# Optimization experiments

Hardware: AMD Instinct MI355X
Metric: run time of the kernel (lower is better)

The kernel has to match this reference:

```python
import jax, jax.numpy as jnp
import numpy as np

# lower-triangular <-> 3x3 symmetric matrix index maps (match torch_lotri2mat/mat2lotri)
LOTRI = np.array([[0, 1, 3], [1, 2, 4], [3, 4, 5]])
ROWS = np.array([0, 1, 1, 2, 2, 2])
COLS = np.array([0, 0, 1, 0, 1, 2])
NUM_NEWTON_ITERS = 6


def det3(A):
    # A: (N,3,3)
    return (A[:, 0, 0] * (A[:, 1, 1] * A[:, 2, 2] - A[:, 1, 2] * A[:, 2, 1])
            - A[:, 0, 1] * (A[:, 1, 0] * A[:, 2, 2] - A[:, 1, 2] * A[:, 2, 0])
            + A[:, 0, 2] * (A[:, 1, 0] * A[:, 2, 1] - A[:, 1, 1] * A[:, 2, 0]))


def inv3(A):
    # closed-form 3x3 inverse via adjugate; A: (N,3,3)
    c00 = A[:, 1, 1] * A[:, 2, 2] - A[:, 1, 2] * A[:, 2, 1]
    c01 = A[:, 0, 2] * A[:, 2, 1] - A[:, 0, 1] * A[:, 2, 2]
    c02 = A[:, 0, 1] * A[:, 1, 2] - A[:, 0, 2] * A[:, 1, 1]
    c10 = A[:, 1, 2] * A[:, 2, 0] - A[:, 1, 0] * A[:, 2, 2]
    c11 = A[:, 0, 0] * A[:, 2, 2] - A[:, 0, 2] * A[:, 2, 0]
    c12 = A[:, 0, 2] * A[:, 1, 0] - A[:, 0, 0] * A[:, 1, 2]
    c20 = A[:, 1, 0] * A[:, 2, 1] - A[:, 1, 1] * A[:, 2, 0]
    c21 = A[:, 0, 1] * A[:, 2, 0] - A[:, 0, 0] * A[:, 2, 1]
    c22 = A[:, 0, 0] * A[:, 1, 1] - A[:, 0, 1] * A[:, 1, 0]
    adj = jnp.stack([jnp.stack([c00, c01, c02], -1),
                     jnp.stack([c10, c11, c12], -1),
                     jnp.stack([c20, c21, c22], -1)], -2)  # (N,3,3)
    det = (A[:, 0, 0] * c00 + A[:, 0, 1] * c10 + A[:, 0, 2] * c20)
    return adj / det[:, None, None]


def trilinear_warp(img, ddf):
    # img: (B,C,H,W,D), ddf: (B,3,H,W,D) in voxel units; border padding (clamped corners)
    B, C, H, W, D = img.shape
    base = jnp.stack(jnp.meshgrid(jnp.arange(H), jnp.arange(W), jnp.arange(D),
                                  indexing='ij'), 0).astype(img.dtype)  # (3,H,W,D)
    coords = base[None] + ddf                                           # (B,3,H,W,D)
    c0 = jnp.floor(coords)
    frac = coords - c0
    c0i = c0.astype(jnp.int32)
    dims = jnp.array([H, W, D], jnp.int32).reshape(1, 3, 1, 1, 1)
    lo = jnp.clip(c0i, 0, dims - 1)
    hi = jnp.clip(c0i + 1, 0, dims - 1)
    imgf = img.reshape(B, C, H * W * D)

    def gather(xi, yi, zi):
        lin = (xi * W + yi) * D + zi                      # (B,H,W,D)
        idx = jnp.broadcast_to(lin.reshape(B, 1, -1), (B, C, H * W * D))
        return jnp.take_along_axis(imgf, idx, axis=2).reshape(B, C, H, W, D)

    fx, fy, fz = frac[:, 0, None], frac[:, 1, None], frac[:, 2, None]  # (B,1,H,W,D)
    x0, y0, z0 = lo[:, 0], lo[:, 1], lo[:, 2]
    x1, y1, z1 = hi[:, 0], hi[:, 1], hi[:, 2]
    out = jnp.zeros_like(img)
    for xi, wx in ((x0, 1.0 - fx), (x1, fx)):
        for yi, wy in ((y0, 1.0 - fy), (y1, fy)):
            for zi, wz in ((z0, 1.0 - fz), (z1, fz)):
                out = out + wx * wy * wz * gather(xi, yi, zi)
    return out


def ddf_jacobian(ddf):
    # Jacobian of the deformation phi(x)=x+ddf(x): J = I + d(ddf_i)/dx_j (central differences)
    rows = []
    for i in range(3):
        g = jnp.gradient(ddf[:, i], axis=(1, 2, 3))  # list of 3 arrays (B,H,W,D)
        rows.append(jnp.stack(g, axis=1))
    J = jnp.stack(rows, axis=1)                      # (B,3,3,H,W,D)
    eye = jnp.eye(3, dtype=ddf.dtype).reshape(1, 3, 3, 1, 1, 1)
    return J + eye


def newton_polar_det(X, n_iters):
    # Newton iteration for polar decomposition with determinant scaling
    U = X
    for _ in range(n_iters):
        zeta = jnp.abs(det3(U)) ** (-1.0 / 3.0)
        zU = zeta[:, None, None] * U
        U = 0.5 * (zU + inv3(jnp.swapaxes(zU, -1, -2)))
    return U


def setup_inputs() -> dict:
    key = jax.random.key(0)
    k1, k2 = jax.random.split(key)
    B, H, W, D = 2, 128, 128, 128
    dti = jax.random.normal(k1, (B, 6, H, W, D), dtype=jnp.float32)
    # smooth, realistic displacement field so J = I + grad(ddf) is well-conditioned
    g = jnp.stack(jnp.meshgrid(jnp.arange(H), jnp.arange(W), jnp.arange(D),
                               indexing='ij'), 0).astype(jnp.float32) / H  # (3,H,W,D)
    two_pi = 2.0 * jnp.pi
    amp = 2.0
    ddf = amp * jnp.stack([jnp.sin(two_pi * (g[0] + 0.5 * g[1])),
                           jnp.cos(two_pi * (g[1] + 0.5 * g[2])),
                           jnp.sin(two_pi * (g[2] + 0.5 * g[0]))], 0)  # (3,H,W,D)
    ddf = jnp.broadcast_to(ddf[None], (B, 3, H, W, D))
    ddf = ddf + 0.02 * jax.random.normal(k2, (B, 3, H, W, D), dtype=jnp.float32)
    return {"dti": dti, "ddf": ddf}


def reference(dti, ddf):
    B, _, H, W, D = dti.shape
    # 1) warp the lower-triangular DTI with trilinear interpolation (border padding)
    warped_lotri = trilinear_warp(dti, ddf)              # (B,6,H,W,D)
    # 2) lotri -> 3x3 symmetric matrices, absorb spatial dims
    Dmat = warped_lotri[:, LOTRI]                        # (B,3,3,H,W,D)
    Dns = Dmat.transpose(0, 3, 4, 5, 1, 2).reshape(-1, 3, 3)
    # 3) Jacobian of DDF, absorb spatial dims
    J = ddf_jacobian(ddf)                                # (B,3,3,H,W,D)
    Jns = J.transpose(0, 3, 4, 5, 1, 2).reshape(-1, 3, 3)
    # 4) rotation from polar decomposition (Newton, det scaling)
    R = newton_polar_det(Jns, NUM_NEWTON_ITERS)          # (N,3,3)
    # 5) finite-strain reorientation: R^T D R per voxel
    out_ns = jnp.einsum('nji,njk,nkl->nil', R, Dns, R)
    # 6) expand spatial dims, mat -> lotri
    out_mat = out_ns.reshape(B, H, W, D, 3, 3).transpose(0, 4, 5, 1, 2, 3)
    return out_mat[:, ROWS, COLS]                        # (B,6,H,W,D)
```

## Files before the change

### kernel.cpp

```cpp
#include <hip/hip_runtime.h>

#define NH 128
#define NW 128
#define ND 128
#define HWD (NH * NW * ND)
#define NB 2

__global__ __launch_bounds__(256) void warp_dti_kernel(
    const float* __restrict__ dti,
    const float* __restrict__ ddf,
    float* __restrict__ out)
{
    const int tid = blockIdx.x * 256 + threadIdx.x;
    const int d = tid & (ND - 1);
    const int w = (tid >> 7) & (NW - 1);
    const int h = (tid >> 14) & (NH - 1);
    const int b = tid >> 21;
    const int sp = tid & (HWD - 1);

    const float* dbase = ddf + b * 3 * HWD;

    float u[3];
#pragma unroll
    for (int c = 0; c < 3; ++c) u[c] = dbase[c * HWD + sp];

    float A[3][3];
#pragma unroll
    for (int c = 0; c < 3; ++c) {
        const float* p = dbase + c * HWD;
        float gh, gw, gd;
        if (h == 0)           gh = p[sp + NW * ND] - u[c];
        else if (h == NH - 1) gh = u[c] - p[sp - NW * ND];
        else                  gh = 0.5f * (p[sp + NW * ND] - p[sp - NW * ND]);
        if (w == 0)           gw = p[sp + ND] - u[c];
        else if (w == NW - 1) gw = u[c] - p[sp - ND];
        else                  gw = 0.5f * (p[sp + ND] - p[sp - ND]);
        if (d == 0)           gd = p[sp + 1] - u[c];
        else if (d == ND - 1) gd = u[c] - p[sp - 1];
        else                  gd = 0.5f * (p[sp + 1] - p[sp - 1]);
        A[c][0] = gh; A[c][1] = gw; A[c][2] = gd;
    }
    A[0][0] += 1.0f; A[1][1] += 1.0f; A[2][2] += 1.0f;

    float U[3][3];
#pragma unroll
    for (int i = 0; i < 3; ++i)
#pragma unroll
        for (int j = 0; j < 3; ++j) U[i][j] = A[i][j];

#pragma unroll
    for (int it = 0; it < 6; ++it) {
        float c00 = U[1][1]*U[2][2] - U[1][2]*U[2][1];
        float c01 = U[0][2]*U[2][1] - U[0][1]*U[2][2];
        float c02 = U[0][1]*U[1][2] - U[0][2]*U[1][1];
        float c10 = U[1][2]*U[2][0] - U[1][0]*U[2][2];
        float c11 = U[0][0]*U[2][2] - U[0][2]*U[2][0];
        float c12 = U[0][2]*U[1][0] - U[0][0]*U[1][2];
        float c20 = U[1][0]*U[2][1] - U[1][1]*U[2][0];
        float c21 = U[0][1]*U[2][0] - U[0][0]*U[2][1];
        float c22 = U[0][0]*U[1][1] - U[0][1]*U[1][0];
        float det = U[0][0]*c00 + U[0][1]*c10 + U[0][2]*c20;

        float l    = __log2f(fabsf(det));
        float zeta = __builtin_amdgcn_exp2f(-0.33333333333333333f * l);
        float s    = copysignf(zeta * zeta, det);
        float hz = 0.5f * zeta;
        float hs = 0.5f * s;

        float n00 = hz*U[0][0] + c00*hs;
        float n01 = hz*U[0][1] + c10*hs;
        float n02 = hz*U[0][2] + c20*hs;
        float n10 = hz*U[1][0] + c01*hs;
        float n11 = hz*U[1][1] + c11*hs;
        float n12 = hz*U[1][2] + c21*hs;
        float n20 = hz*U[2][0] + c02*hs;
        float n21 = hz*U[2][1] + c12*hs;
        float n22 = hz*U[2][2] + c22*hs;
        U[0][0]=n00; U[0][1]=n01; U[0][2]=n02;
        U[1][0]=n10; U[1][1]=n11; U[1][2]=n12;
        U[2][0]=n20; U[2][1]=n21; U[2][2]=n22;
    }

    float cx = (float)h + u[0];
    float cy = (float)w + u[1];
    float cz = (float)d + u[2];
    float flx = floorf(cx), fly = floorf(cy), flz = floorf(cz);
    float fx = cx - flx, fy = cy - fly, fz = cz - flz;
    int x0 = (int)flx, y0 = (int)fly, z0 = (int)flz;
    int xi[2], yi[2], zi[2];
    xi[0] = min(max(x0,     0), NH - 1); xi[1] = min(max(x0 + 1, 0), NH - 1);
    yi[0] = min(max(y0,     0), NW - 1); yi[1] = min(max(y0 + 1, 0), NW - 1);
    zi[0] = min(max(z0,     0), ND - 1); zi[1] = min(max(z0 + 1, 0), ND - 1);
    float wx[2] = {1.0f - fx, fx};
    float wy[2] = {1.0f - fy, fy};
    float wz[2] = {1.0f - fz, fz};

    const float* img = dti + b * 6 * HWD;
    float acc[6] = {0.f, 0.f, 0.f, 0.f, 0.f, 0.f};
#pragma unroll
    for (int i = 0; i < 2; ++i) {
#pragma unroll
        for (int j = 0; j < 2; ++j) {
            int rowoff = (xi[i] * NW + yi[j]) * ND;
            float wij = wx[i] * wy[j];
#pragma unroll
            for (int k = 0; k < 2; ++k) {
                float wgt = wij * wz[k];
                int lin = rowoff + zi[k];
#pragma unroll
                for (int ch = 0; ch < 6; ++ch)
                    acc[ch] += wgt * img[ch * HWD + lin];
            }
        }
    }

    float Dm[3][3];
    Dm[0][0] = acc[0]; Dm[0][1] = acc[1]; Dm[0][2] = acc[3];
    Dm[1][0] = acc[1]; Dm[1][1] = acc[2]; Dm[1][2] = acc[4];
    Dm[2][0] = acc[3]; Dm[2][1] = acc[4]; Dm[2][2] = acc[5];

    float M[3][3];
#pragma unroll
    for (int i = 0; i < 3; ++i)
#pragma unroll
        for (int k = 0; k < 3; ++k)
            M[i][k] = U[0][i]*Dm[0][k] + U[1][i]*Dm[1][k] + U[2][i]*Dm[2][k];

    float T00 = M[0][0]*U[0][0] + M[0][1]*U[1][0] + M[0][2]*U[2][0];
    float T10 = M[1][0]*U[0][0] + M[1][1]*U[1][0] + M[1][2]*U[2][0];
    float T11 = M[1][0]*U[0][1] + M[1][1]*U[1][1] + M[1][2]*U[2][1];
    float T20 = M[2][0]*U[0][0] + M[2][1]*U[1][0] + M[2][2]*U[2][0];
    float T21 = M[2][0]*U[0][1] + M[2][1]*U[1][1] + M[2][2]*U[2][1];
    float T22 = M[2][0]*U[0][2] + M[2][1]*U[1][2] + M[2][2]*U[2][2];

    float* obase = out + b * 6 * HWD + sp;
    obase[0]       = T00;
    obase[HWD]     = T10;
    obase[2 * HWD] = T11;
    obase[3 * HWD] = T20;
    obase[4 * HWD] = T21;
    obase[5 * HWD] = T22;
}

extern "C" void kernel_launch(void* const* d_in, const int* in_sizes, int n_in,
                              void* d_out, int out_size, void* d_ws, size_t ws_size,
                              hipStream_t stream) {
    const float* dti = (const float*)d_in[0];
    const float* ddf = (const float*)d_in[1];
    float* o = (float*)d_out;
    const int n = NB * HWD;
    warp_dti_kernel<<<n / 256, 256, 0, stream>>>(dti, ddf, o);
}
```

Baseline: 308.6 us.

## Issue all gathers before Newton iterations and use branchless stencil offsets

Moves the trilinear coordinate computation and all 48 DTI gathers ahead of the polar-decomposition Newton loop, fenced by a sched_barrier, so gather memory latency overlaps the ALU-heavy iterations. The boundary if/else chains in the Jacobian stencil become branchless clamped offsets with a scale factor, and index math is derived from block and thread ids separately. It costs many more live registers (48 gathered values plus stencil neighbours), which can lower occupancy.

```diff
diff --git a/kernel.cpp b/kernel.cpp
--- a/kernel.cpp
+++ b/kernel.cpp
@@ -4,6 +4,7 @@
 #define NW 128
 #define ND 128
 #define HWD (NH * NW * ND)
+#define NWD (NW * ND)
 #define NB 2
 
 __global__ __launch_bounds__(256) void warp_dti_kernel(
@@ -11,42 +12,81 @@
     const float* __restrict__ ddf,
     float* __restrict__ out)
 {
-    const int tid = blockIdx.x * 256 + threadIdx.x;
-    const int d = tid & (ND - 1);
-    const int w = (tid >> 7) & (NW - 1);
-    const int h = (tid >> 14) & (NH - 1);
-    const int b = tid >> 21;
-    const int sp = tid & (HWD - 1);
+    const int blk   = blockIdx.x;
+    const int b     = blk >> 13;
+    const int blkin = blk & 8191;
+    const int tid   = threadIdx.x;
+    const int sp    = (blkin << 8) | tid;
+    const int d     = tid & (ND - 1);
+    const int w     = ((blkin & 63) << 1) | (tid >> 7);
+    const int h     = blkin >> 6;
 
-    const float* dbase = ddf + b * 3 * HWD;
+    const int dbase = b * 3 * HWD;
 
-    float u[3];
-#pragma unroll
-    for (int c = 0; c < 3; ++c) u[c] = dbase[c * HWD + sp];
+    const int oh_m = (h > 0)      ? -NWD : 0;
+    const int oh_p = (h < NH - 1) ?  NWD : 0;
+    const int ow_m = (w > 0)      ? -ND  : 0;
+    const int ow_p = (w < NW - 1) ?  ND  : 0;
+    const int od_m = (d > 0)      ? -1   : 0;
+    const int od_p = (d < ND - 1) ?  1   : 0;
 
-    float A[3][3];
+    float uc[3], hm[3], hp[3], wm[3], wp[3], dm[3], dp[3];
 #pragma unroll
     for (int c = 0; c < 3; ++c) {
-        const float* p = dbase + c * HWD;
-        float gh, gw, gd;
-        if (h == 0)           gh = p[sp + NW * ND] - u[c];
-        else if (h == NH - 1) gh = u[c] - p[sp - NW * ND];
-        else                  gh = 0.5f * (p[sp + NW * ND] - p[sp - NW * ND]);
-        if (w == 0)           gw = p[sp + ND] - u[c];
-        else if (w == NW - 1) gw = u[c] - p[sp - ND];
-        else                  gw = 0.5f * (p[sp + ND] - p[sp - ND]);
-        if (d == 0)           gd = p[sp + 1] - u[c];
-        else if (d == ND - 1) gd = u[c] - p[sp - 1];
-        else                  gd = 0.5f * (p[sp + 1] - p[sp - 1]);
-        A[c][0] = gh; A[c][1] = gw; A[c][2] = gd;
+        const float* p = ddf + dbase + c * HWD;
+        uc[c] = p[sp];
     }
-    A[0][0] += 1.0f; A[1][1] += 1.0f; A[2][2] += 1.0f;
+#pragma unroll
+    for (int c = 0; c < 3; ++c) {
+        const float* p = ddf + dbase + c * HWD;
+        hm[c] = p[sp + oh_m];  hp[c] = p[sp + oh_p];
+        wm[c] = p[sp + ow_m];  wp[c] = p[sp + ow_p];
+        dm[c] = p[sp + od_m];  dp[c] = p[sp + od_p];
+    }
+
+    const float cx = (float)h + uc[0];
+    const float cy = (float)w + uc[1];
+    const float cz = (float)d + uc[2];
+    const float flx = floorf(cx), fly = floorf(cy), flz = floorf(cz);
+    const float fx = cx - flx, fy = cy - fly, fz = cz - flz;
+    const int x0 = (int)flx, y0 = (int)fly, z0 = (int)flz;
+    const int xa = min(max(x0,     0), NH - 1), xb = min(max(x0 + 1, 0), NH - 1);
+    const int ya = min(max(y0,     0), NW - 1), yb = min(max(y0 + 1, 0), NW - 1);
+    const int za = min(max(z0,     0), ND - 1), zb = min(max(z0 + 1, 0), ND - 1);
+
+    const int raa = (xa * NW + ya) * ND;
+    const int rab = (xa * NW + yb) * ND;
+    const int rba = (xb * NW + ya) * ND;
+    const int rbb = (xb * NW + yb) * ND;
+
+    int lin[8];
+    lin[0] = raa + za; lin[1] = raa + zb;
+    lin[2] = rab + za; lin[3] = rab + zb;
+    lin[4] = rba + za; lin[5] = rba + zb;
+    lin[6] = rbb + za; lin[7] = rbb + zb;
+
+    const int ibase = b * 6 * HWD;
+    float g[8][6];
+#pragma unroll
+    for (int c = 0; c < 8; ++c)
+#pragma unroll
+        for (int ch = 0; ch < 6; ++ch)
+            g[c][ch] = dti[ibase + ch * HWD + lin[c]];
+
+    __builtin_amdgcn_sched_barrier(0);
+
+    const float sh = (oh_m == 0 || oh_p == 0) ? 1.0f : 0.5f;
+    const float sw = (ow_m == 0 || ow_p == 0) ? 1.0f : 0.5f;
+    const float sd = (od_m == 0 || od_p == 0) ? 1.0f : 0.5f;
 
     float U[3][3];
 #pragma unroll
-    for (int i = 0; i < 3; ++i)
-#pragma unroll
-        for (int j = 0; j < 3; ++j) U[i][j] = A[i][j];
+    for (int c = 0; c < 3; ++c) {
+        U[c][0] = sh * (hp[c] - hm[c]);
+        U[c][1] = sw * (wp[c] - wm[c]);
+        U[c][2] = sd * (dp[c] - dm[c]);
+    }
+    U[0][0] += 1.0f; U[1][1] += 1.0f; U[2][2] += 1.0f;
 
 #pragma unroll
     for (int it = 0; it < 6; ++it) {
@@ -81,38 +121,19 @@
         U[2][0]=n20; U[2][1]=n21; U[2][2]=n22;
     }
 
-    float cx = (float)h + u[0];
-    float cy = (float)w + u[1];
-    float cz = (float)d + u[2];
-    float flx = floorf(cx), fly = floorf(cy), flz = floorf(cz);
-    float fx = cx - flx, fy = cy - fly, fz = cz - flz;
-    int x0 = (int)flx, y0 = (int)fly, z0 = (int)flz;
-    int xi[2], yi[2], zi[2];
-    xi[0] = min(max(x0,     0), NH - 1); xi[1] = min(max(x0 + 1, 0), NH - 1);
-    yi[0] = min(max(y0,     0), NW - 1); yi[1] = min(max(y0 + 1, 0), NW - 1);
-    zi[0] = min(max(z0,     0), ND - 1); zi[1] = min(max(z0 + 1, 0), ND - 1);
-    float wx[2] = {1.0f - fx, fx};
-    float wy[2] = {1.0f - fy, fy};
-    float wz[2] = {1.0f - fz, fz};
+    const float wxa = 1.0f - fx, wya = 1.0f - fy, wza = 1.0f - fz;
+    float wc[8];
+    wc[0] = (wxa * wya) * wza;  wc[1] = (wxa * wya) * fz;
+    wc[2] = (wxa * fy)  * wza;  wc[3] = (wxa * fy)  * fz;
+    wc[4] = (fx  * wya) * wza;  wc[5] = (fx  * wya) * fz;
+    wc[6] = (fx  * fy)  * wza;  wc[7] = (fx  * fy)  * fz;
 
-    const float* img = dti + b * 6 * HWD;
     float acc[6] = {0.f, 0.f, 0.f, 0.f, 0.f, 0.f};
 #pragma unroll
-    for (int i = 0; i < 2; ++i) {
+    for (int c = 0; c < 8; ++c)
 #pragma unroll
-        for (int j = 0; j < 2; ++j) {
-            int rowoff = (xi[i] * NW + yi[j]) * ND;
-            float wij = wx[i] * wy[j];
-#pragma unroll
-            for (int k = 0; k < 2; ++k) {
-                float wgt = wij * wz[k];
-                int lin = rowoff + zi[k];
-#pragma unroll
-                for (int ch = 0; ch < 6; ++ch)
-                    acc[ch] += wgt * img[ch * HWD + lin];
-            }
-        }
-    }
+        for (int ch = 0; ch < 6; ++ch)
+            acc[ch] = fmaf(wc[c], g[c][ch], acc[ch]);
 
     float Dm[3][3];
     Dm[0][0] = acc[0]; Dm[0][1] = acc[1]; Dm[0][2] = acc[3];
@@ -133,13 +154,13 @@
     float T21 = M[2][0]*U[0][1] + M[2][1]*U[1][1] + M[2][2]*U[2][1];
     float T22 = M[2][0]*U[0][2] + M[2][1]*U[1][2] + M[2][2]*U[2][2];
 
-    float* obase = out + b * 6 * HWD + sp;
-    obase[0]       = T00;
-    obase[HWD]     = T10;
-    obase[2 * HWD] = T11;
-    obase[3 * HWD] = T20;
-    obase[4 * HWD] = T21;
-    obase[5 * HWD] = T22;
+    const int obase = b * 6 * HWD;
+    out[obase + 0 * HWD + sp] = T00;
+    out[obase + 1 * HWD + sp] = T10;
+    out[obase + 2 * HWD + sp] = T11;
+    out[obase + 3 * HWD + sp] = T20;
+    out[obase + 4 * HWD + sp] = T21;
+    out[obase + 5 * HWD + sp] = T22;
 }
 
 extern "C" void kernel_launch(void* const* d_in, const int* in_sizes, int n_in,
```

Measured after the change: 299.3 us. 3.0% less time.

## Process two voxels per thread with software-pipelined inline-asm loads and paired z gathers

Applied to the files above, without the earlier changes.

Each thread now handles two voxels 64 planes apart in h. Global loads are issued through inline asm with manual vmcnt waits and sched barriers, so the gather for one voxel and the stencil loads for the other overlap with the Newton polar iterations. The trilinear z-pair is fetched as a single dwordx2 load, with edge-aware weights that reproduce clamping. Boundary gradients use offset and scale selection instead of branches. In exchange, register pressure rises, and the hand-set waitcnt counts are fragile if the compiler reorders or adds memory operations.

```diff
diff --git a/kernel.cpp b/kernel.cpp
--- a/kernel.cpp
+++ b/kernel.cpp
@@ -4,50 +4,17 @@
 #define NW 128
 #define ND 128
 #define HWD (NH * NW * ND)
+#define NWD (NW * ND)
 #define NB 2
 
-__global__ __launch_bounds__(256) void warp_dti_kernel(
-    const float* __restrict__ dti,
-    const float* __restrict__ ddf,
-    float* __restrict__ out)
-{
-    const int tid = blockIdx.x * 256 + threadIdx.x;
-    const int d = tid & (ND - 1);
-    const int w = (tid >> 7) & (NW - 1);
-    const int h = (tid >> 14) & (NH - 1);
-    const int b = tid >> 21;
-    const int sp = tid & (HWD - 1);
-
-    const float* dbase = ddf + b * 3 * HWD;
-
-    float u[3];
-#pragma unroll
-    for (int c = 0; c < 3; ++c) u[c] = dbase[c * HWD + sp];
-
-    float A[3][3];
-#pragma unroll
-    for (int c = 0; c < 3; ++c) {
-        const float* p = dbase + c * HWD;
-        float gh, gw, gd;
-        if (h == 0)           gh = p[sp + NW * ND] - u[c];
-        else if (h == NH - 1) gh = u[c] - p[sp - NW * ND];
-        else                  gh = 0.5f * (p[sp + NW * ND] - p[sp - NW * ND]);
-        if (w == 0)           gw = p[sp + ND] - u[c];
-        else if (w == NW - 1) gw = u[c] - p[sp - ND];
-        else                  gw = 0.5f * (p[sp + ND] - p[sp - ND]);
-        if (d == 0)           gd = p[sp + 1] - u[c];
-        else if (d == ND - 1) gd = u[c] - p[sp - 1];
-        else                  gd = 0.5f * (p[sp + 1] - p[sp - 1]);
-        A[c][0] = gh; A[c][1] = gw; A[c][2] = gd;
-    }
-    A[0][0] += 1.0f; A[1][1] += 1.0f; A[2][2] += 1.0f;
-
-    float U[3][3];
-#pragma unroll
-    for (int i = 0; i < 3; ++i)
-#pragma unroll
-        for (int j = 0; j < 3; ++j) U[i][j] = A[i][j];
-
+typedef float f32x2 __attribute__((ext_vector_type(2)));
+
+#define SB() __builtin_amdgcn_sched_barrier(0)
+#define LD1(dst, voff, base) asm volatile("global_load_dword %0, %1, %2" : "=v"(dst) : "v"(voff), "s"(base))
+#define LD2(dst, voff, base) asm volatile("global_load_dwordx2 %0, %1, %2" : "=v"(dst) : "v"(voff), "s"(base))
+#define TOUCH(x) asm volatile("" : "+v"(x))
+
+__device__ __forceinline__ void newton6(float U[3][3]) {
 #pragma unroll
     for (int it = 0; it < 6; ++it) {
         float c00 = U[1][1]*U[2][2] - U[1][2]*U[2][1];
@@ -80,66 +47,215 @@
         U[1][0]=n10; U[1][1]=n11; U[1][2]=n12;
         U[2][0]=n20; U[2][1]=n21; U[2][2]=n22;
     }
-
-    float cx = (float)h + u[0];
-    float cy = (float)w + u[1];
-    float cz = (float)d + u[2];
+}
+
+__device__ __forceinline__ void corner_setup(float cx, float cy, float cz,
+                                             unsigned vo[4], float wA[4], float wB[4])
+{
     float flx = floorf(cx), fly = floorf(cy), flz = floorf(cz);
     float fx = cx - flx, fy = cy - fly, fz = cz - flz;
     int x0 = (int)flx, y0 = (int)fly, z0 = (int)flz;
-    int xi[2], yi[2], zi[2];
-    xi[0] = min(max(x0,     0), NH - 1); xi[1] = min(max(x0 + 1, 0), NH - 1);
-    yi[0] = min(max(y0,     0), NW - 1); yi[1] = min(max(y0 + 1, 0), NW - 1);
-    zi[0] = min(max(z0,     0), ND - 1); zi[1] = min(max(z0 + 1, 0), ND - 1);
-    float wx[2] = {1.0f - fx, fx};
-    float wy[2] = {1.0f - fy, fy};
-    float wz[2] = {1.0f - fz, fz};
-
-    const float* img = dti + b * 6 * HWD;
-    float acc[6] = {0.f, 0.f, 0.f, 0.f, 0.f, 0.f};
-#pragma unroll
-    for (int i = 0; i < 2; ++i) {
-#pragma unroll
-        for (int j = 0; j < 2; ++j) {
-            int rowoff = (xi[i] * NW + yi[j]) * ND;
-            float wij = wx[i] * wy[j];
-#pragma unroll
-            for (int k = 0; k < 2; ++k) {
-                float wgt = wij * wz[k];
-                int lin = rowoff + zi[k];
-#pragma unroll
-                for (int ch = 0; ch < 6; ++ch)
-                    acc[ch] += wgt * img[ch * HWD + lin];
-            }
+    int xa = min(max(x0,     0), NH - 1), xb = min(max(x0 + 1, 0), NH - 1);
+    int ya = min(max(y0,     0), NW - 1), yb = min(max(y0 + 1, 0), NW - 1);
+    int pa = min(max(z0, 0), ND - 2);
+    vo[0] = (unsigned)(((xa * NW + ya) * ND) + pa) * 4u;
+    vo[1] = (unsigned)(((xa * NW + yb) * ND) + pa) * 4u;
+    vo[2] = (unsigned)(((xb * NW + ya) * ND) + pa) * 4u;
+    vo[3] = (unsigned)(((xb * NW + yb) * ND) + pa) * 4u;
+    float wza = 1.0f - fz, wzb = fz;
+    float wv0 = ((z0 <= ND - 2) ? wza : 0.0f) + ((z0 <= -1) ? wzb : 0.0f);
+    float wv1 = ((z0 >= ND - 1) ? wza : 0.0f) + ((z0 >=  0) ? wzb : 0.0f);
+    float wxa = 1.0f - fx, wya = 1.0f - fy;
+    float w0 = wxa * wya, w1 = wxa * fy, w2 = fx * wya, w3 = fx * fy;
+    wA[0] = w0 * wv0; wA[1] = w1 * wv0; wA[2] = w2 * wv0; wA[3] = w3 * wv0;
+    wB[0] = w0 * wv1; wB[1] = w1 * wv1; wB[2] = w2 * wv1; wB[3] = w3 * wv1;
+}
+
+__global__ __launch_bounds__(256) void warp_dti_kernel(
+    const float* __restrict__ dti,
+    const float* __restrict__ ddf,
+    float* __restrict__ out)
+{
+    const int blk   = blockIdx.x;
+    const int b     = blk >> 12;
+    const int blkin = blk & 4095;
+    const int tid   = threadIdx.x;
+    const int d     = tid & (ND - 1);
+    const int w     = ((blkin & 63) << 1) | (tid >> 7);
+    const int hA    = blkin >> 6;
+    const int hB    = hA + 64;
+    const int spA   = (hA << 14) | (w << 7) | d;
+    const unsigned vA = (unsigned)spA * 4u;
+    const unsigned vB = vA + (unsigned)(64 * NWD * 4);
+
+    const float* dch[3];
+    const float* tch[6];
+#pragma unroll
+    for (int c = 0; c < 3; ++c) dch[c] = ddf + (size_t)(b * 3 + c) * HWD;
+#pragma unroll
+    for (int c = 0; c < 6; ++c) tch[c] = dti + (size_t)(b * 6 + c) * HWD;
+
+    const unsigned owm = (w > 0)      ? (unsigned)(-(ND * 4)) : 0u;
+    const unsigned owp = (w < NW - 1) ? (unsigned)(ND * 4)    : 0u;
+    const unsigned odm = (d > 0)      ? (unsigned)-4 : 0u;
+    const unsigned odp = (d < ND - 1) ? 4u            : 0u;
+    const unsigned vrmA = vA + ((hA > 0) ? (unsigned)(-(NWD * 4)) : 0u);
+    const unsigned vrpA = vA + (unsigned)(NWD * 4);
+    const unsigned vrmB = vB - (unsigned)(NWD * 4);
+    const unsigned vrpB = vB + ((hB < NH - 1) ? (unsigned)(NWD * 4) : 0u);
+
+    const float shA = (hA > 0)              ? 0.5f : 1.0f;
+    const float shB = (hB < NH - 1)         ? 0.5f : 1.0f;
+    const float sw  = (w > 0 && w < NW - 1) ? 0.5f : 1.0f;
+    const float sd  = (d > 0 && d < ND - 1) ? 0.5f : 1.0f;
+
+    float a_c[3];
+#pragma unroll
+    for (int c = 0; c < 3; ++c) LD1(a_c[c], vA, dch[c]);
+    float a_rm[3], a_rp[3], a_wm[3], a_wp[3], a_dm[3], a_dp[3];
+#pragma unroll
+    for (int c = 0; c < 3; ++c) {
+        LD1(a_rm[c], vrmA,     dch[c]); LD1(a_rp[c], vrpA,     dch[c]);
+        LD1(a_wm[c], vA + owm, dch[c]); LD1(a_wp[c], vA + owp, dch[c]);
+        LD1(a_dm[c], vA + odm, dch[c]); LD1(a_dp[c], vA + odp, dch[c]);
+    }
+
+    asm volatile("s_waitcnt vmcnt(18)" ::: "memory"); SB();
+#pragma unroll
+    for (int c = 0; c < 3; ++c) TOUCH(a_c[c]);
+    unsigned voA[4]; float wA0[4], wB0[4];
+    corner_setup((float)hA + a_c[0], (float)w + a_c[1], (float)d + a_c[2], voA, wA0, wB0);
+    SB();
+
+    f32x2 gA[6][4];
+#pragma unroll
+    for (int ch = 0; ch < 6; ++ch)
+#pragma unroll
+        for (int c = 0; c < 4; ++c) LD2(gA[ch][c], voA[c], tch[ch]);
+
+    asm volatile("s_waitcnt vmcnt(24)" ::: "memory"); SB();
+#pragma unroll
+    for (int c = 0; c < 3; ++c) {
+        TOUCH(a_rm[c]); TOUCH(a_rp[c]); TOUCH(a_wm[c]);
+        TOUCH(a_wp[c]); TOUCH(a_dm[c]); TOUCH(a_dp[c]);
+    }
+    float UA[3][3];
+#pragma unroll
+    for (int c = 0; c < 3; ++c) {
+        UA[c][0] = shA * (a_rp[c] - a_rm[c]);
+        UA[c][1] = sw  * (a_wp[c] - a_wm[c]);
+        UA[c][2] = sd  * (a_dp[c] - a_dm[c]);
+    }
+    UA[0][0] += 1.0f; UA[1][1] += 1.0f; UA[2][2] += 1.0f;
+    SB();
+
+    float b_c[3];
+#pragma unroll
+    for (int c = 0; c < 3; ++c) LD1(b_c[c], vB, dch[c]);
+    float b_rm[3], b_rp[3], b_wm[3], b_wp[3], b_dm[3], b_dp[3];
+#pragma unroll
+    for (int c = 0; c < 3; ++c) {
+        LD1(b_rm[c], vrmB,     dch[c]); LD1(b_rp[c], vrpB,     dch[c]);
+        LD1(b_wm[c], vB + owm, dch[c]); LD1(b_wp[c], vB + owp, dch[c]);
+        LD1(b_dm[c], vB + odm, dch[c]); LD1(b_dp[c], vB + odp, dch[c]);
+    }
+    SB();
+
+    newton6(UA);
+
+    asm volatile("s_waitcnt vmcnt(21)" ::: "memory"); SB();
+#pragma unroll
+    for (int ch = 0; ch < 6; ++ch)
+#pragma unroll
+        for (int c = 0; c < 4; ++c) TOUCH(gA[ch][c]);
+    float accA[6] = {0.f, 0.f, 0.f, 0.f, 0.f, 0.f};
+#pragma unroll
+    for (int c = 0; c < 4; ++c)
+#pragma unroll
+        for (int ch = 0; ch < 6; ++ch)
+            accA[ch] = fmaf(wA0[c], gA[ch][c].x, fmaf(wB0[c], gA[ch][c].y, accA[ch]));
+    SB();
+
+    asm volatile("s_waitcnt vmcnt(18)" ::: "memory"); SB();
+#pragma unroll
+    for (int c = 0; c < 3; ++c) TOUCH(b_c[c]);
+    unsigned voB[4]; float wA1[4], wB1[4];
+    corner_setup((float)hB + b_c[0], (float)w + b_c[1], (float)d + b_c[2], voB, wA1, wB1);
+    SB();
+
+    f32x2 gB[6][4];
+#pragma unroll
+    for (int ch = 0; ch < 6; ++ch)
+#pragma unroll
+        for (int c = 0; c < 4; ++c) LD2(gB[ch][c], voB[c], tch[ch]);
+
+    asm volatile("s_waitcnt vmcnt(24)" ::: "memory"); SB();
+#pragma unroll
+    for (int c = 0; c < 3; ++c) {
+        TOUCH(b_rm[c]); TOUCH(b_rp[c]); TOUCH(b_wm[c]);
+        TOUCH(b_wp[c]); TOUCH(b_dm[c]); TOUCH(b_dp[c]);
+    }
+    float UB[3][3];
+#pragma unroll
+    for (int c = 0; c < 3; ++c) {
+        UB[c][0] = shB * (b_rp[c] - b_rm[c]);
+        UB[c][1] = sw  * (b_wp[c] - b_wm[c]);
+        UB[c][2] = sd  * (b_dp[c] - b_dm[c]);
+    }
+    UB[0][0] += 1.0f; UB[1][1] += 1.0f; UB[2][2] += 1.0f;
+    SB();
+
+    {
+        float Dm00 = accA[0], Dm01 = accA[1], Dm02 = accA[3];
+        float Dm11 = accA[2], Dm12 = accA[4], Dm22 = accA[5];
+        float M[3][3];
+#pragma unroll
+        for (int i = 0; i < 3; ++i) {
+            M[i][0] = UA[0][i]*Dm00 + UA[1][i]*Dm01 + UA[2][i]*Dm02;
+            M[i][1] = UA[0][i]*Dm01 + UA[1][i]*Dm11 + UA[2][i]*Dm12;
+            M[i][2] = UA[0][i]*Dm02 + UA[1][i]*Dm12 + UA[2][i]*Dm22;
         }
-    }
-
-    float Dm[3][3];
-    Dm[0][0] = acc[0]; Dm[0][1] = acc[1]; Dm[0][2] = acc[3];
-    Dm[1][0] = acc[1]; Dm[1][1] = acc[2]; Dm[1][2] = acc[4];
-    Dm[2][0] = acc[3]; Dm[2][1] = acc[4]; Dm[2][2] = acc[5];
-
-    float M[3][3];
-#pragma unroll
-    for (int i = 0; i < 3; ++i)
-#pragma unroll
-        for (int k = 0; k < 3; ++k)
-            M[i][k] = U[0][i]*Dm[0][k] + U[1][i]*Dm[1][k] + U[2][i]*Dm[2][k];
-
-    float T00 = M[0][0]*U[0][0] + M[0][1]*U[1][0] + M[0][2]*U[2][0];
-    float T10 = M[1][0]*U[0][0] + M[1][1]*U[1][0] + M[1][2]*U[2][0];
-    float T11 = M[1][0]*U[0][1] + M[1][1]*U[1][1] + M[1][2]*U[2][1];
-    float T20 = M[2][0]*U[0][0] + M[2][1]*U[1][0] + M[2][2]*U[2][0];
-    float T21 = M[2][0]*U[0][1] + M[2][1]*U[1][1] + M[2][2]*U[2][1];
-    float T22 = M[2][0]*U[0][2] + M[2][1]*U[1][2] + M[2][2]*U[2][2];
-
-    float* obase = out + b * 6 * HWD + sp;
-    obase[0]       = T00;
-    obase[HWD]     = T10;
-    obase[2 * HWD] = T11;
-    obase[3 * HWD] = T20;
-    obase[4 * HWD] = T21;
-    obase[5 * HWD] = T22;
+        float* obase = out + (size_t)b * 6 * HWD + spA;
+        obase[0]       = M[0][0]*UA[0][0] + M[0][1]*UA[1][0] + M[0][2]*UA[2][0];
+        obase[HWD]     = M[1][0]*UA[0][0] + M[1][1]*UA[1][0] + M[1][2]*UA[2][0];
+        obase[2 * HWD] = M[1][0]*UA[0][1] + M[1][1]*UA[1][1] + M[1][2]*UA[2][1];
+        obase[3 * HWD] = M[2][0]*UA[0][0] + M[2][1]*UA[1][0] + M[2][2]*UA[2][0];
+        obase[4 * HWD] = M[2][0]*UA[0][1] + M[2][1]*UA[1][1] + M[2][2]*UA[2][1];
+        obase[5 * HWD] = M[2][0]*UA[0][2] + M[2][1]*UA[1][2] + M[2][2]*UA[2][2];
+    }
+
+    newton6(UB);
+
+    asm volatile("s_waitcnt vmcnt(0)" ::: "memory"); SB();
+#pragma unroll
+    for (int ch = 0; ch < 6; ++ch)
+#pragma unroll
+        for (int c = 0; c < 4; ++c) TOUCH(gB[ch][c]);
+    float accB[6] = {0.f, 0.f, 0.f, 0.f, 0.f, 0.f};
+#pragma unroll
+    for (int c = 0; c < 4; ++c)
+#pragma unroll
+        for (int ch = 0; ch < 6; ++ch)
+            accB[ch] = fmaf(wA1[c], gB[ch][c].x, fmaf(wB1[c], gB[ch][c].y, accB[ch]));
+
+    {
+        float Dm00 = accB[0], Dm01 = accB[1], Dm02 = accB[3];
+        float Dm11 = accB[2], Dm12 = accB[4], Dm22 = accB[5];
+        float M[3][3];
+#pragma unroll
+        for (int i = 0; i < 3; ++i) {
+            M[i][0] = UB[0][i]*Dm00 + UB[1][i]*Dm01 + UB[2][i]*Dm02;
+            M[i][1] = UB[0][i]*Dm01 + UB[1][i]*Dm11 + UB[2][i]*Dm12;
+            M[i][2] = UB[0][i]*Dm02 + UB[1][i]*Dm12 + UB[2][i]*Dm22;
+        }
+        float* obase = out + (size_t)b * 6 * HWD + spA + 64 * NWD;
+        obase[0]       = M[0][0]*UB[0][0] + M[0][1]*UB[1][0] + M[0][2]*UB[2][0];
+        obase[HWD]     = M[1][0]*UB[0][0] + M[1][1]*UB[1][0] + M[1][2]*UB[2][0];
+        obase[2 * HWD] = M[1][0]*UB[0][1] + M[1][1]*UB[1][1] + M[1][2]*UB[2][1];
+        obase[3 * HWD] = M[2][0]*UB[0][0] + M[2][1]*UB[1][0] + M[2][2]*UB[2][0];
+        obase[4 * HWD] = M[2][0]*UB[0][1] + M[2][1]*UB[1][1] + M[2][2]*UB[2][1];
+        obase[5 * HWD] = M[2][0]*UB[0][2] + M[2][1]*UB[1][2] + M[2][2]*UB[2][2];
+    }
 }
 
 extern "C" void kernel_launch(void* const* d_in, const int* in_sizes, int n_in,
@@ -148,6 +264,6 @@
     const float* dti = (const float*)d_in[0];
     const float* ddf = (const float*)d_in[1];
     float* o = (float*)d_out;
-    const int n = NB * HWD;
-    warp_dti_kernel<<<n / 256, 256, 0, stream>>>(dti, ddf, o);
-}
+    const int nblocks = NB * 64 * 64;
+    warp_dti_kernel<<<nblocks, 256, 0, stream>>>(dti, ddf, o);
+}
```

After: 273.9 us. 1.13x faster.
